# Kernel tuning notes

Measured on AMD Instinct MI355X. Metric: run time of the kernel, lower is better.

Reference implementation:

```python
import jax, jax.numpy as jnp
import numpy as np

N = 16384      # patches per slide
D = 1024       # inputd (hard-coded by attmil's Linear(1024, hd1))
HD = 512       # hd
HD2 = 256      # hd // 2
TOPK = 100     # torch.arange(100) after descending sort == top-100
R = 0.3
M_SEL = int(R * N)  # 4915 salient patches


def _l2norm(v, axis):
    # matches F.normalize(p=2, eps=1e-12)
    return v / jnp.maximum(jnp.linalg.norm(v, axis=axis, keepdims=True), 1e-12)


def setup_inputs() -> dict:
    key = jax.random.key(0)
    ks = jax.random.split(key, 12)
    def p(k, shape, scale=0.02):
        return jax.random.normal(k, shape, dtype=jnp.float32) * scale
    return {
        "x0": jax.random.normal(ks[0], (1, N, D), dtype=jnp.float32),
        "x1": jax.random.normal(ks[1], (1, N, D), dtype=jnp.float32),
        "Wq": p(ks[2], (D, HD)),  "bq": jnp.zeros((HD,), jnp.float32),
        "Wk": p(ks[3], (D, HD)),  "bk": jnp.zeros((HD,), jnp.float32),
        "W1": p(ks[4], (D, HD)),  "b1": jnp.zeros((HD,), jnp.float32),
        "Wv": p(ks[5], (HD, HD2)), "bv": jnp.zeros((HD2,), jnp.float32),
        "Wu": p(ks[6], (HD, HD2)), "bu": jnp.zeros((HD2,), jnp.float32),
        "Wa": p(ks[7], (HD2, 1)),  "ba": jnp.zeros((1,), jnp.float32),
        "Wc": p(ks[8], (HD, 1)),   "bc": jnp.zeros((1,), jnp.float32),
    }


def reference(x0, x1, Wq, bq, Wk, bk, W1, b1, Wv, bv, Wu, bu, Wa, ba, Wc, bc):
    # query/key projections with tanh
    q = jnp.tanh(x0 @ Wq + bq)                       # [1, N, HD]
    k = jnp.tanh(x1 @ Wk + bk)                       # [1, N, HD]
    qn = _l2norm(q, -1)
    kn = _l2norm(k, -1)
    A = jnp.einsum('bnd,bmd->bnm', qn, kn)           # cosine sims [1, N, N]
    # descending sort + index_select(arange(100)) == top-100 per row
    topv, _ = jax.lax.top_k(A, TOPK)                 # [1, N, 100]
    A1 = jnp.mean(topv, axis=-1)                     # saliency [1, N]
    # ascending sort of saliency; take first M_SEL indices (batch 0)
    sortidx = jnp.argsort(A1[0])                     # [N]
    sel = sortidx[:M_SEL]                            # [M_SEL]
    sal = x0[:, sel, :]                              # gather [1, M_SEL, D]
    # gated-attention MIL (attmil)
    feat = jax.nn.relu(sal @ W1 + b1)                # [1, M, HD]
    av = jnp.tanh(feat @ Wv + bv)                    # [1, M, HD2]
    au = jax.nn.sigmoid(feat @ Wu + bu)              # [1, M, HD2]
    att = (av * au) @ Wa + ba                        # [1, M, 1]
    att = jax.nn.softmax(att.transpose(0, 2, 1), axis=2)  # [1, 1, M]
    Mv = (att @ feat).reshape(-1, HD)                # [1, HD]
    Y_prob = Mv @ Wc + bc                            # [1, 1]
    return Y_prob, att
```

## Files before the change

kernel.cpp:

```cpp
#include <hip/hip_runtime.h>

typedef unsigned short u16;
typedef unsigned int u32;
typedef unsigned long long u64;

typedef __attribute__((ext_vector_type(8))) short bf16x8;
typedef __attribute__((ext_vector_type(4))) float f32x4;

__device__ __forceinline__ u16 f2b(float f) {
  u32 u = __float_as_uint(f);
  u32 r = (u + 0x7fffu + ((u >> 16) & 1u)) >> 16;
  return (u16)r;
}
__device__ __forceinline__ float b2f(u16 h) {
  return __uint_as_float(((u32)h) << 16);
}
__device__ __forceinline__ float key2f(u32 k) {
  u16 kk = (u16)k;
  u16 bits = (kk & 0x8000) ? (u16)(kk ^ 0x8000) : (u16)(~kk);
  return b2f(bits);
}
__device__ __forceinline__ u64 makekey(float f, int i) {
  u32 u = __float_as_uint(f);
  u = (u & 0x80000000u) ? ~u : (u | 0x80000000u);
  return ((u64)u << 32) | (u32)i;
}

__device__ __forceinline__ void gload16(const void* g, void* l) {
  __builtin_amdgcn_global_load_lds((const __attribute__((address_space(1))) void*)g,
                                   (__attribute__((address_space(3))) void*)l, 16, 0, 0);
}

__global__ __launch_bounds__(256) void conv_k(const float* __restrict__ s,
                                              u16* __restrict__ d, int n8) {
  int i = blockIdx.x * 256 + threadIdx.x;
  if (i >= n8) return;
  const float4* s4 = reinterpret_cast<const float4*>(s);
  float4 f0 = s4[i * 2], f1 = s4[i * 2 + 1];
  __align__(16) u16 t[8];
  t[0] = f2b(f0.x); t[1] = f2b(f0.y); t[2] = f2b(f0.z); t[3] = f2b(f0.w);
  t[4] = f2b(f1.x); t[5] = f2b(f1.y); t[6] = f2b(f1.z); t[7] = f2b(f1.w);
  reinterpret_cast<uint4*>(d)[i] = *reinterpret_cast<uint4*>(t);
}

__global__ __launch_bounds__(256) void convt_k(const float* __restrict__ W,
                                               u16* __restrict__ Wt, int K, int Nc) {
  __shared__ float t[32][33];
  int k0 = blockIdx.x * 32, n0 = blockIdx.y * 32;
  int c = threadIdx.x & 31, r4 = threadIdx.x >> 5;
#pragma unroll
  for (int i = 0; i < 4; ++i) {
    int r = r4 + i * 8;
    t[r][c] = W[(size_t)(k0 + r) * Nc + n0 + c];
  }
  __syncthreads();
#pragma unroll
  for (int i = 0; i < 4; ++i) {
    int r = r4 + i * 8;
    Wt[(size_t)(n0 + r) * K + k0 + c] = f2b(t[c][r]);
  }
}

template <int MODE>
__global__ __launch_bounds__(512, 2) void mm8_k(
    const u16* __restrict__ A, const u16* __restrict__ B, int K, int Mbase,
    int mtiles, const float* __restrict__ rs, const float* __restrict__ cs,
    const float* __restrict__ bias, u16* __restrict__ out, int ldc) {
  __shared__ u16 lds[2][2][2][128][32];
  int tid = threadIdx.x, lane = tid & 63, wid = tid >> 6;
  int wm = wid >> 2, wn = wid & 3;
  int rsel = lane & 15, rgrp = lane >> 4;

  int nwg = gridDim.x * gridDim.y;
  int fid = blockIdx.y * gridDim.x + blockIdx.x;
  int chunk = nwg >> 3;
  int s = (fid & 7) * chunk + (fid >> 3);
  int mtile = s % mtiles, ntile = s / mtiles;
  int mrow0 = Mbase + mtile * 256;
  int ncol0 = ntile * 256;

  int strow = wid * 16 + (lane >> 2);
  int stch = (lane & 3) ^ ((lane >> 3) & 3);

  auto stage = [&](int sbuf, int smat, int shalf, int kt) {
    int grow = (smat ? ncol0 : mrow0) + shalf * 128 + strow;
    const u16* g = (smat ? B : A) + (size_t)grow * K + kt * 32 + stch * 8;
    gload16(g, &lds[sbuf][smat][shalf][wid * 16][0]);
  };

  f32x4 acc[4][4][2] = {};
  bf16x8 afr[4], bfr[2][2];

  auto rdA = [&](int buf, int ah) {
#pragma unroll
    for (int mf = 0; mf < 4; ++mf) {
      int row = wm * 64 + mf * 16 + rsel;
      afr[mf] = *reinterpret_cast<const bf16x8*>(
          &lds[buf][0][ah][row][(rgrp ^ ((row >> 1) & 3)) * 8]);
    }
  };
  auto rdB = [&](int buf) {
#pragma unroll
    for (int bh = 0; bh < 2; ++bh)
#pragma unroll
      for (int nf = 0; nf < 2; ++nf) {
        int row = wn * 32 + nf * 16 + rsel;
        bfr[bh][nf] = *reinterpret_cast<const bf16x8*>(
            &lds[buf][1][bh][row][(rgrp ^ ((row >> 1) & 3)) * 8]);
      }
  };
  auto mm = [&](int ah) {
#pragma unroll
    for (int bh = 0; bh < 2; ++bh)
#pragma unroll
      for (int mf = 0; mf < 4; ++mf)
#pragma unroll
        for (int nf = 0; nf < 2; ++nf)
          acc[ah * 2 + bh][mf][nf] = __builtin_amdgcn_mfma_f32_16x16x32_bf16(
              afr[mf], bfr[bh][nf], acc[ah * 2 + bh][mf][nf], 0, 0, 0);
  };

  int nkt = K / 32;
  stage(0, 0, 0, 0); stage(0, 1, 0, 0); stage(0, 1, 1, 0); stage(0, 0, 1, 0);
  stage(1, 0, 0, 1); stage(1, 1, 0, 1);
  asm volatile("s_waitcnt vmcnt(2)" ::: "memory");
  __builtin_amdgcn_s_barrier();

  for (int j = 0; j < nkt / 2; ++j) {
    int t1 = 2 * j + 1;
    int t2 = (2 * j + 2 < nkt) ? 2 * j + 2 : nkt - 1;
    int t3 = (2 * j + 3 < nkt) ? 2 * j + 3 : nkt - 1;
    rdB(0); rdA(0, 0);
    stage(1, 1, 1, t1); stage(1, 0, 1, t1);
    __builtin_amdgcn_s_setprio(1); mm(0); __builtin_amdgcn_s_setprio(0);
    __builtin_amdgcn_s_barrier();
    rdA(0, 1);
    stage(0, 0, 0, t2); stage(0, 1, 0, t2);
    __builtin_amdgcn_s_setprio(1); mm(1); __builtin_amdgcn_s_setprio(0);
    asm volatile("s_waitcnt vmcnt(2)" ::: "memory");
    __builtin_amdgcn_s_barrier();
    rdB(1); rdA(1, 0);
    stage(0, 1, 1, t2); stage(0, 0, 1, t2);
    __builtin_amdgcn_s_setprio(1); mm(0); __builtin_amdgcn_s_setprio(0);
    __builtin_amdgcn_s_barrier();
    rdA(1, 1);
    stage(1, 0, 0, t3); stage(1, 1, 0, t3);
    __builtin_amdgcn_s_setprio(1); mm(1); __builtin_amdgcn_s_setprio(0);
    asm volatile("s_waitcnt vmcnt(2)" ::: "memory");
    __builtin_amdgcn_s_barrier();
  }

#pragma unroll
  for (int q = 0; q < 4; ++q)
#pragma unroll
    for (int mf = 0; mf < 4; ++mf)
#pragma unroll
      for (int nf = 0; nf < 2; ++nf)
#pragma unroll
        for (int r = 0; r < 4; ++r) {
          int rl = mtile * 256 + (q >> 1) * 128 + wm * 64 + mf * 16 + rgrp * 4 + r;
          int cl = ncol0 + (q & 1) * 128 + wn * 32 + nf * 16 + rsel;
          float v = acc[q][mf][nf][r] * rs[Mbase + rl] * cs[cl];
          out[(size_t)rl * ldc + cl] = f2b(v);
        }
}

__global__ __launch_bounds__(512, 2) void mm8p_k(
    const u16* __restrict__ A, const u16* __restrict__ B, int K, int mtiles,
    const float* __restrict__ bias, u16* __restrict__ out, int ldc,
    const u16* A2, const u16* B2, const float* bias2, u16* out2) {
  if (blockIdx.z) { A = A2; B = B2; bias = bias2; out = out2; }
  __shared__ u16 lds[3][3][128][32];
  int tid = threadIdx.x, lane = tid & 63, wid = tid >> 6;
  int wm = wid >> 2, wn = wid & 3;
  int rsel = lane & 15, rgrp = lane >> 4;

  int nwg = gridDim.x * gridDim.y;
  int fid = blockIdx.y * gridDim.x + blockIdx.x;
  int chunk = nwg >> 3;
  int s = (fid & 7) * chunk + (fid >> 3);
  int mtile = s % mtiles, ntile = s / mtiles;
  int mrow0 = mtile * 128;
  int ncol0 = ntile * 256;

  int strow = wid * 16 + (lane >> 2);
  int stch = (lane & 3) ^ ((lane >> 3) & 3);

  auto stage = [&](int sbuf, int slot, int kt) {
    int grow = (slot == 0 ? mrow0 : ncol0 + (slot - 1) * 128) + strow;
    const u16* g = (slot == 0 ? A : B) + (size_t)grow * K + kt * 32 + stch * 8;
    gload16(g, &lds[sbuf][slot][wid * 16][0]);
  };

  f32x4 acc[2][4][2] = {};
  bf16x8 afr[4], bfr[2][2];

  auto rdAll = [&](int buf) {
#pragma unroll
    for (int mf = 0; mf < 4; ++mf) {
      int row = wm * 64 + mf * 16 + rsel;
      afr[mf] = *reinterpret_cast<const bf16x8*>(
          &lds[buf][0][row][(rgrp ^ ((row >> 1) & 3)) * 8]);
    }
#pragma unroll
    for (int bh = 0; bh < 2; ++bh)
#pragma unroll
      for (int nf = 0; nf < 2; ++nf) {
        int row = wn * 32 + nf * 16 + rsel;
        bfr[bh][nf] = *reinterpret_cast<const bf16x8*>(
            &lds[buf][1 + bh][row][(rgrp ^ ((row >> 1) & 3)) * 8]);
      }
  };
  auto mm16 = [&]() {
#pragma unroll
    for (int bh = 0; bh < 2; ++bh)
#pragma unroll
      for (int mf = 0; mf < 4; ++mf)
#pragma unroll
        for (int nf = 0; nf < 2; ++nf)
          acc[bh][mf][nf] = __builtin_amdgcn_mfma_f32_16x16x32_bf16(
              afr[mf], bfr[bh][nf], acc[bh][mf][nf], 0, 0, 0);
  };

  int nkt = K / 32;
  stage(0, 0, 0); stage(0, 1, 0); stage(0, 2, 0);
  stage(1, 0, 1); stage(1, 1, 1); stage(1, 2, 1);
  asm volatile("s_waitcnt vmcnt(3)" ::: "memory");
  __builtin_amdgcn_s_barrier();

  int cur = 0;
  for (int t = 0; t < nkt; ++t) {
    rdAll(cur);
    int tn = (t + 2 < nkt) ? t + 2 : nkt - 1;
    int nb = cur + 2; if (nb >= 3) nb -= 3;
    stage(nb, 0, tn); stage(nb, 1, tn); stage(nb, 2, tn);
    __builtin_amdgcn_s_setprio(1); mm16(); __builtin_amdgcn_s_setprio(0);
    asm volatile("s_waitcnt vmcnt(3)" ::: "memory");
    __builtin_amdgcn_s_barrier();
    cur = (cur + 1 == 3) ? 0 : cur + 1;
  }

#pragma unroll
  for (int bh = 0; bh < 2; ++bh)
#pragma unroll
    for (int mf = 0; mf < 4; ++mf)
#pragma unroll
      for (int nf = 0; nf < 2; ++nf)
#pragma unroll
        for (int r = 0; r < 4; ++r) {
          int rl = mrow0 + wm * 64 + mf * 16 + rgrp * 4 + r;
          int cl = ncol0 + bh * 128 + wn * 32 + nf * 16 + rsel;
          float v = tanhf(acc[bh][mf][nf][r] + bias[cl]);
          out[(size_t)rl * ldc + cl] = f2b(v);
        }
}

#define TILE 128
#define BK 32

template <int MODE>
__global__ __launch_bounds__(256) void gemm2_k(
    const u16* __restrict__ Abf, const u16* __restrict__ Bbf, int lda, int ldb,
    int K, int Mreal, const float* __restrict__ bias,
    const u32* __restrict__ gidx, float* __restrict__ outf,
    u16* __restrict__ outb, int ldc,
    const u16* Abf2, const u16* Bbf2, const float* bias2,
    float* outf2, u16* outb2) {
  if (blockIdx.z) {
    if (Abf2) Abf = Abf2;
    if (Bbf2) Bbf = Bbf2;
    if (bias2) bias = bias2;
    if (outf2) outf = outf2;
    if (outb2) outb = outb2;
  }
  __shared__ u16 As[2][TILE][BK];
  __shared__ u16 Bs[2][TILE][BK];
  int tid = threadIdx.x, lane = tid & 63, wid = tid >> 6;
  int mt = blockIdx.x, nt2 = blockIdx.y;
  int row0 = (wid >> 1) * 64, col0 = (wid & 1) * 64;

  int scol = (lane & 3) * 8;
  const u16* gA[2];
  const u16* gB[2];
#pragma unroll
  for (int h = 0; h < 2; ++h) {
    int rA = (wid * 2 + h) * 16 + (lane >> 2);
    int grow = mt * TILE + rA;
    int arow;
    if (MODE == 2) arow = (int)gidx[grow < Mreal ? grow : 0];
    else arow = grow;
    gA[h] = Abf + (size_t)arow * lda + scol;
    int bcol = nt2 * TILE + rA;
    gB[h] = Bbf + (size_t)bcol * ldb + scol;
  }

  auto stage = [&](int buf, int kt) {
#pragma unroll
    for (int h = 0; h < 2; ++h) {
      gload16(gA[h] + kt, &As[buf][(wid * 2 + h) * 16][0]);
      gload16(gB[h] + kt, &Bs[buf][(wid * 2 + h) * 16][0]);
    }
  };

  f32x4 acc[4][4] = {};
  int k8 = 8 * (lane >> 4), rsel = lane & 15;
  int nkt = K / BK;

  stage(0, 0);
  __syncthreads();
  int cur = 0;
  for (int t = 0; t < nkt; ++t) {
    if (t + 1 < nkt) stage(cur ^ 1, (t + 1) * BK);
    bf16x8 a[4], b[4];
#pragma unroll
    for (int m = 0; m < 4; ++m)
      a[m] = *reinterpret_cast<const bf16x8*>(&As[cur][row0 + m * 16 + rsel][k8]);
#pragma unroll
    for (int n = 0; n < 4; ++n)
      b[n] = *reinterpret_cast<const bf16x8*>(&Bs[cur][col0 + n * 16 + rsel][k8]);
    __builtin_amdgcn_s_setprio(1);
#pragma unroll
    for (int m = 0; m < 4; ++m)
#pragma unroll
      for (int n = 0; n < 4; ++n)
        acc[m][n] = __builtin_amdgcn_mfma_f32_16x16x32_bf16(a[m], b[n], acc[m][n], 0, 0, 0);
    __builtin_amdgcn_s_setprio(0);
    __syncthreads();
    cur ^= 1;
  }

  int rgrp = lane >> 4, csel = lane & 15;
#pragma unroll
  for (int m = 0; m < 4; ++m)
#pragma unroll
    for (int n = 0; n < 4; ++n)
#pragma unroll
      for (int r = 0; r < 4; ++r) {
        int grow = mt * TILE + row0 + m * 16 + rgrp * 4 + r;
        int gcol = nt2 * TILE + col0 + n * 16 + csel;
        float v = acc[m][n][r];
        if (MODE == 2) {
          if (grow < Mreal) {
            v = fmaxf(v + bias[gcol], 0.f);
            outf[(size_t)grow * ldc + gcol] = v;
            outb[(size_t)grow * ldc + gcol] = f2b(v);
          }
        } else {
          if (grow < Mreal) outf[(size_t)grow * ldc + gcol] = v + bias[gcol];
        }
      }
}

__global__ __launch_bounds__(256) void norm_k(const u16* __restrict__ qb,
                                              float* __restrict__ inv, int rows, int dcols) {
  int gw = (int)((blockIdx.x * 256 + threadIdx.x) >> 6);
  int lane = threadIdx.x & 63;
  if (gw >= rows) return;
  const u16* r = qb + (size_t)gw * dcols;
  float s = 0.f;
  for (int c = lane; c < dcols; c += 64) { float v = b2f(r[c]); s += v * v; }
  for (int o = 32; o; o >>= 1) s += __shfl_down(s, o);
  if (lane == 0) inv[gw] = 1.f / fmaxf(sqrtf(s), 1e-12f);
}

__global__ __launch_bounds__(256) void topk_k(const u16* __restrict__ Ablk,
                                              float* __restrict__ A1, int rowbase) {
  __shared__ u32 hist[16][257];
  __shared__ u32 histlo[8][257];
  __shared__ u32 chist[256];
  __shared__ u32 sfx[257];
  __shared__ float wsfx[257];
  __shared__ float wsum[4];
  __shared__ int s_bhi;
  __shared__ u32 s_above;
  __shared__ float s_tail;
  int row = blockIdx.x, tid = threadIdx.x, wid = tid >> 6, lane = tid & 63;
  const uint4* src4 = reinterpret_cast<const uint4*>(Ablk + (size_t)row * 16384);
  uint4 regs[8];
#pragma unroll
  for (int v = 0; v < 8; ++v) regs[v] = src4[v * 256 + tid];
  for (int i = tid; i < 16 * 257; i += 256) (&hist[0][0])[i] = 0;
  for (int i = tid; i < 8 * 257; i += 256) (&histlo[0][0])[i] = 0;
#pragma unroll
  for (int v = 0; v < 8; ++v) {
    u32* w = reinterpret_cast<u32*>(&regs[v]);
#pragma unroll
    for (int h = 0; h < 4; ++h) {
      u32 x = w[h];
      u16 lo = (u16)x, hi = (u16)(x >> 16);
      lo = (lo & 0x8000) ? (u16)(~lo) : (u16)(lo | 0x8000);
      hi = (hi & 0x8000) ? (u16)(~hi) : (u16)(hi | 0x8000);
      w[h] = (u32)lo | ((u32)hi << 16);
    }
  }
  __syncthreads();

  u32* myh = &hist[lane & 15][0];
#pragma unroll
  for (int v = 0; v < 8; ++v) {
    const u32* w = reinterpret_cast<const u32*>(&regs[v]);
#pragma unroll
    for (int h = 0; h < 4; ++h) {
      atomicAdd(&myh[(w[h] >> 8) & 0xffu], 1u);
      atomicAdd(&myh[w[h] >> 24], 1u);
    }
  }
  __syncthreads();
  {
    u32 c = 0;
#pragma unroll
    for (int j = 0; j < 16; ++j) c += hist[j][tid];
    sfx[tid] = c;
    if (tid == 0) sfx[256] = 0;
  }
  __syncthreads();
#pragma unroll
  for (int st = 1; st < 256; st <<= 1) {
    u32 add = (tid + st < 256) ? sfx[tid + st] : 0u;
    __syncthreads();
    sfx[tid] += add;
    __syncthreads();
  }
  if (sfx[tid] >= 100u && sfx[tid + 1] < 100u) {
    s_bhi = tid;
    s_above = sfx[tid + 1];
  }
  __syncthreads();
  u32 bhi = (u32)s_bhi, above = s_above;

  u32* myl = &histlo[lane & 7][0];
  float lsum = 0.f;
#pragma unroll
  for (int v = 0; v < 8; ++v) {
    const u32* w = reinterpret_cast<const u32*>(&regs[v]);
#pragma unroll
    for (int h = 0; h < 4; ++h) {
#pragma unroll
      for (int half = 0; half < 2; ++half) {
        u32 k = (w[h] >> (half * 16)) & 0xffffu;
        u32 hb = k >> 8;
        if (hb > bhi) lsum += key2f(k);
        else if (hb == bhi) atomicAdd(&myl[k & 0xffu], 1u);
      }
    }
  }
  for (int o = 32; o; o >>= 1) lsum += __shfl_down(lsum, o);
  if (lane == 0) wsum[wid] = lsum;
  __syncthreads();
  {
    u32 c = 0;
#pragma unroll
    for (int j = 0; j < 8; ++j) c += histlo[j][tid];
    chist[tid] = c;
    sfx[tid] = c;
    wsfx[tid] = (float)c * key2f((bhi << 8) | (u32)tid);
    if (tid == 0) { sfx[256] = 0; wsfx[256] = 0.f; }
  }
  __syncthreads();
#pragma unroll
  for (int st = 1; st < 256; st <<= 1) {
    u32 a = (tid + st < 256) ? sfx[tid + st] : 0u;
    float b = (tid + st < 256) ? wsfx[tid + st] : 0.f;
    __syncthreads();
    sfx[tid] += a;
    wsfx[tid] += b;
    __syncthreads();
  }
  {
    u32 need = 100u - above;
    if (sfx[tid] >= need && sfx[tid + 1] < need) {
      s_tail = wsfx[tid + 1] +
               (float)(need - sfx[tid + 1]) * key2f((bhi << 8) | (u32)tid);
    }
  }
  __syncthreads();
  if (tid == 0) {
    float tot = wsum[0] + wsum[1] + wsum[2] + wsum[3];
    A1[rowbase + row] = (tot + s_tail) * 0.01f;
  }
}

__global__ __launch_bounds__(256) void rankpart_k(const float* __restrict__ A1,
                                                  u32* __restrict__ rank) {
  __shared__ u64 tile[2048];
  int i = blockIdx.x * 256 + threadIdx.x;
  int t0 = blockIdx.y * 2048;
  u64 my = makekey(A1[i], i);
  for (int j = threadIdx.x; j < 2048; j += 256) tile[j] = makekey(A1[t0 + j], t0 + j);
  __syncthreads();
  u32 r = 0;
  for (int j = 0; j < 2048; ++j) r += (tile[j] < my) ? 1u : 0u;
  atomicAdd(&rank[i], r);
}

__global__ __launch_bounds__(256) void scatter_k(const u32* __restrict__ rank,
                                                 u32* __restrict__ sortidx) {
  int i = blockIdx.x * 256 + threadIdx.x;
  sortidx[rank[i]] = (u32)i;
}

__global__ __launch_bounds__(256) void attlogit_k(const float* __restrict__ avr,
                                                  const float* __restrict__ aur,
                                                  const float* __restrict__ featf,
                                                  const float* __restrict__ Wa,
                                                  const float* __restrict__ Wc,
                                                  float* __restrict__ z, float* __restrict__ g,
                                                  int M) {
  int gw = (int)((blockIdx.x * 256 + threadIdx.x) >> 6);
  int lane = threadIdx.x & 63;
  if (gw >= M) return;
  float s = 0.f;
  for (int c = lane; c < 256; c += 64) {
    float a = tanhf(avr[(size_t)gw * 256 + c]);
    float u = 1.f / (1.f + expf(-aur[(size_t)gw * 256 + c]));
    s += a * u * Wa[c];
  }
  float t = 0.f;
  for (int c = lane; c < 512; c += 64) t += featf[(size_t)gw * 512 + c] * Wc[c];
  for (int o = 32; o; o >>= 1) {
    s += __shfl_down(s, o);
    t += __shfl_down(t, o);
  }
  if (lane == 0) {
    z[gw] = s;
    g[gw] = t;
  }
}

__global__ __launch_bounds__(1024) void final_k(const float* __restrict__ z,
                                                const float* __restrict__ g,
                                                const float* __restrict__ bc,
                                                float* __restrict__ out, int M) {
  __shared__ float sred[16], s1[16], s2[16];
  int tid = threadIdx.x, lane = tid & 63, w = tid >> 6;
  float m = -1e30f;
  for (int i = tid; i < M; i += 1024) m = fmaxf(m, z[i]);
  for (int o = 32; o; o >>= 1) m = fmaxf(m, __shfl_down(m, o));
  if (lane == 0) sred[w] = m;
  __syncthreads();
  if (w == 0) {
    float t = (lane < 16) ? sred[lane] : -1e30f;
    for (int o = 8; o; o >>= 1) t = fmaxf(t, __shfl_down(t, o));
    if (lane == 0) sred[0] = t;
  }
  __syncthreads();
  m = sred[0];
  float se = 0.f, sg = 0.f;
  for (int i = tid; i < M; i += 1024) {
    float e = expf(z[i] - m);
    se += e;
    sg += e * g[i];
  }
  for (int o = 32; o; o >>= 1) {
    se += __shfl_down(se, o);
    sg += __shfl_down(sg, o);
  }
  if (lane == 0) {
    s1[w] = se;
    s2[w] = sg;
  }
  __syncthreads();
  if (w == 0) {
    float a = (lane < 16) ? s1[lane] : 0.f;
    float b = (lane < 16) ? s2[lane] : 0.f;
    for (int o = 8; o; o >>= 1) {
      a += __shfl_down(a, o);
      b += __shfl_down(b, o);
    }
    if (lane == 0) {
      s1[0] = a;
      s2[0] = b;
    }
  }
  __syncthreads();
  float inv = 1.f / s1[0];
  for (int i = tid; i < M; i += 1024) out[1 + i] = expf(z[i] - m) * inv;
  if (tid == 0) out[0] = s2[0] * inv + bc[0];
}

extern "C" void kernel_launch(void* const* d_in, const int* in_sizes, int n_in,
                              void* d_out, int out_size, void* d_ws, size_t ws_size,
                              hipStream_t stream) {
  const int N = 16384, D = 1024, HD = 512, HD2 = 256, MSEL = 4915;
  const float* x0 = (const float*)d_in[0];
  const float* x1 = (const float*)d_in[1];
  const float* Wq = (const float*)d_in[2];
  const float* bq = (const float*)d_in[3];
  const float* Wk = (const float*)d_in[4];
  const float* bk = (const float*)d_in[5];
  const float* W1 = (const float*)d_in[6];
  const float* b1 = (const float*)d_in[7];
  const float* Wv = (const float*)d_in[8];
  const float* bv = (const float*)d_in[9];
  const float* Wu = (const float*)d_in[10];
  const float* bu = (const float*)d_in[11];
  const float* Wa = (const float*)d_in[12];
  const float* Wc = (const float*)d_in[14];
  const float* bc = (const float*)d_in[15];
  float* out = (float*)d_out;

  char* base = (char*)d_ws;
  size_t off = 0;
  auto alloc = [&](size_t b) {
    void* r = base + off;
    off = (off + b + 255) & ~(size_t)255;
    return r;
  };
  const int MPAD = 4992;
  u16* wqt = (u16*)alloc((size_t)HD * D * 2);
  u16* wkt = (u16*)alloc((size_t)HD * D * 2);
  u16* w1t = (u16*)alloc((size_t)HD * D * 2);
  u16* wvt = (u16*)alloc((size_t)HD2 * HD * 2);
  u16* wut = (u16*)alloc((size_t)HD2 * HD * 2);
  u16* x0b = (u16*)alloc((size_t)N * D * 2);
  u16* x1b = (u16*)alloc((size_t)N * D * 2);
  u16* qb = (u16*)alloc((size_t)N * HD * 2);
  u16* kb = (u16*)alloc((size_t)N * HD * 2);
  float* invq = (float*)alloc((size_t)N * 4);
  float* invk = (float*)alloc((size_t)N * 4);
  float* A1 = (float*)alloc((size_t)N * 4);
  u32* rankbuf = (u32*)alloc((size_t)N * 4);
  u32* sortidx = (u32*)alloc((size_t)N * 4);
  float* featf = (float*)alloc((size_t)MPAD * HD * 4);
  u16* featb = (u16*)alloc((size_t)MPAD * HD * 2);
  float* avr = (float*)alloc((size_t)MPAD * HD2 * 4);
  float* aur = (float*)alloc((size_t)MPAD * HD2 * 4);
  float* zbuf = (float*)alloc((size_t)MPAD * 4);
  float* gbuf = (float*)alloc((size_t)MPAD * 4);
  const int ablk = 2048;
  u16* Ablk = (u16*)alloc((size_t)ablk * N * 2);

  conv_k<<<(N * D / 8 + 255) / 256, 256, 0, stream>>>(x0, x0b, N * D / 8);
  conv_k<<<(N * D / 8 + 255) / 256, 256, 0, stream>>>(x1, x1b, N * D / 8);
  convt_k<<<dim3(D / 32, HD / 32), 256, 0, stream>>>(Wq, wqt, D, HD);
  convt_k<<<dim3(D / 32, HD / 32), 256, 0, stream>>>(Wk, wkt, D, HD);
  convt_k<<<dim3(D / 32, HD / 32), 256, 0, stream>>>(W1, w1t, D, HD);
  convt_k<<<dim3(HD / 32, HD2 / 32), 256, 0, stream>>>(Wv, wvt, HD, HD2);
  convt_k<<<dim3(HD / 32, HD2 / 32), 256, 0, stream>>>(Wu, wut, HD, HD2);

  mm8p_k<<<dim3(4, 64, 2), 512, 0, stream>>>(
      x0b, wqt, D, 128, bq, qb, HD, x1b, wkt, bk, kb);

  norm_k<<<N / 4, 256, 0, stream>>>(qb, invq, N, HD);
  norm_k<<<N / 4, 256, 0, stream>>>(kb, invk, N, HD);

  for (int it = 0; it < N / ablk; ++it) {
    mm8_k<1><<<dim3(8, 64), 512, 0, stream>>>(
        qb, kb, HD, it * ablk, 8, invq, invk, nullptr, Ablk, N);
    topk_k<<<ablk, 256, 0, stream>>>(Ablk, A1, it * ablk);
  }

  hipMemsetAsync(rankbuf, 0, (size_t)N * 4, stream);
  rankpart_k<<<dim3(N / 256, 8), 256, 0, stream>>>(A1, rankbuf);
  scatter_k<<<N / 256, 256, 0, stream>>>(rankbuf, sortidx);

  gemm2_k<2><<<dim3((MSEL + TILE - 1) / TILE, HD / TILE), 256, 0, stream>>>(
      x0b, w1t, D, D, D, MSEL, b1, sortidx, featf, featb, HD,
      nullptr, nullptr, nullptr, nullptr, nullptr);

  gemm2_k<3><<<dim3((MSEL + TILE - 1) / TILE, HD2 / TILE, 2), 256, 0, stream>>>(
      featb, wvt, HD, HD, HD, MSEL, bv, nullptr, avr, nullptr, HD2,
      nullptr, wut, bu, aur, nullptr);

  attlogit_k<<<(MSEL + 3) / 4, 256, 0, stream>>>(avr, aur, featf, Wa, Wc, zbuf, gbuf, MSEL);

  final_k<<<1, 1024, 0, stream>>>(zbuf, gbuf, bc, out, MSEL);
}
```

Measured before the change: 808.2 us.

## Unify GEMM kernels with simpler full-tile double-buffered main loop

```diff
diff --git a/kernel.cpp b/kernel.cpp
--- a/kernel.cpp
+++ b/kernel.cpp
@@ -62,10 +62,12 @@
 }
 
 template <int MODE>
-__global__ __launch_bounds__(512, 2) void mm8_k(
+__global__ __launch_bounds__(512, 2) void mmF_k(
     const u16* __restrict__ A, const u16* __restrict__ B, int K, int Mbase,
     int mtiles, const float* __restrict__ rs, const float* __restrict__ cs,
-    const float* __restrict__ bias, u16* __restrict__ out, int ldc) {
+    const float* __restrict__ bias, u16* __restrict__ out, int ldc,
+    const u16* A2, const u16* B2, const float* bias2, u16* out2) {
+  if (MODE == 0 && blockIdx.z) { A = A2; B = B2; bias = bias2; out = out2; }
   __shared__ u16 lds[2][2][2][128][32];
   int tid = threadIdx.x, lane = tid & 63, wid = tid >> 6;
   int wm = wid >> 2, wn = wid & 3;
@@ -87,19 +89,23 @@
     const u16* g = (smat ? B : A) + (size_t)grow * K + kt * 32 + stch * 8;
     gload16(g, &lds[sbuf][smat][shalf][wid * 16][0]);
   };
+  auto stage4 = [&](int sbuf, int kt) {
+    stage(sbuf, 0, 0, kt); stage(sbuf, 1, 0, kt);
+    stage(sbuf, 0, 1, kt); stage(sbuf, 1, 1, kt);
+  };
 
   f32x4 acc[4][4][2] = {};
-  bf16x8 afr[4], bfr[2][2];
-
-  auto rdA = [&](int buf, int ah) {
-#pragma unroll
-    for (int mf = 0; mf < 4; ++mf) {
-      int row = wm * 64 + mf * 16 + rsel;
-      afr[mf] = *reinterpret_cast<const bf16x8*>(
-          &lds[buf][0][ah][row][(rgrp ^ ((row >> 1) & 3)) * 8]);
-    }
-  };
-  auto rdB = [&](int buf) {
+  bf16x8 afr[2][4], bfr[2][2];
+
+  auto rdAll = [&](int buf) {
+#pragma unroll
+    for (int ah = 0; ah < 2; ++ah)
+#pragma unroll
+      for (int mf = 0; mf < 4; ++mf) {
+        int row = wm * 64 + mf * 16 + rsel;
+        afr[ah][mf] = *reinterpret_cast<const bf16x8*>(
+            &lds[buf][0][ah][row][(rgrp ^ ((row >> 1) & 3)) * 8]);
+      }
 #pragma unroll
     for (int bh = 0; bh < 2; ++bh)
 #pragma unroll
@@ -109,44 +115,36 @@
             &lds[buf][1][bh][row][(rgrp ^ ((row >> 1) & 3)) * 8]);
       }
   };
-  auto mm = [&](int ah) {
-#pragma unroll
-    for (int bh = 0; bh < 2; ++bh)
-#pragma unroll
-      for (int mf = 0; mf < 4; ++mf)
-#pragma unroll
-        for (int nf = 0; nf < 2; ++nf)
-          acc[ah * 2 + bh][mf][nf] = __builtin_amdgcn_mfma_f32_16x16x32_bf16(
-              afr[mf], bfr[bh][nf], acc[ah * 2 + bh][mf][nf], 0, 0, 0);
+  auto mm32 = [&]() {
+#pragma unroll
+    for (int ah = 0; ah < 2; ++ah)
+#pragma unroll
+      for (int bh = 0; bh < 2; ++bh)
+#pragma unroll
+        for (int mf = 0; mf < 4; ++mf)
+#pragma unroll
+          for (int nf = 0; nf < 2; ++nf)
+            acc[ah * 2 + bh][mf][nf] = __builtin_amdgcn_mfma_f32_16x16x32_bf16(
+                afr[ah][mf], bfr[bh][nf], acc[ah * 2 + bh][mf][nf], 0, 0, 0);
   };
 
   int nkt = K / 32;
-  stage(0, 0, 0, 0); stage(0, 1, 0, 0); stage(0, 1, 1, 0); stage(0, 0, 1, 0);
-  stage(1, 0, 0, 1); stage(1, 1, 0, 1);
-  asm volatile("s_waitcnt vmcnt(2)" ::: "memory");
+  stage4(0, 0);
+  stage4(1, 1);
+  asm volatile("s_waitcnt vmcnt(4)" ::: "memory");
   __builtin_amdgcn_s_barrier();
 
-  for (int j = 0; j < nkt / 2; ++j) {
-    int t1 = 2 * j + 1;
-    int t2 = (2 * j + 2 < nkt) ? 2 * j + 2 : nkt - 1;
-    int t3 = (2 * j + 3 < nkt) ? 2 * j + 3 : nkt - 1;
-    rdB(0); rdA(0, 0);
-    stage(1, 1, 1, t1); stage(1, 0, 1, t1);
-    __builtin_amdgcn_s_setprio(1); mm(0); __builtin_amdgcn_s_setprio(0);
+  for (int t = 0; t < nkt; ++t) {
+    int buf = t & 1;
+    rdAll(buf);
+    asm volatile("s_waitcnt lgkmcnt(0)" ::: "memory");
     __builtin_amdgcn_s_barrier();
-    rdA(0, 1);
-    stage(0, 0, 0, t2); stage(0, 1, 0, t2);
-    __builtin_amdgcn_s_setprio(1); mm(1); __builtin_amdgcn_s_setprio(0);
-    asm volatile("s_waitcnt vmcnt(2)" ::: "memory");
-    __builtin_amdgcn_s_barrier();
-    rdB(1); rdA(1, 0);
-    stage(0, 1, 1, t2); stage(0, 0, 1, t2);
-    __builtin_amdgcn_s_setprio(1); mm(0); __builtin_amdgcn_s_setprio(0);
-    __builtin_amdgcn_s_barrier();
-    rdA(1, 1);
-    stage(1, 0, 0, t3); stage(1, 1, 0, t3);
-    __builtin_amdgcn_s_setprio(1); mm(1); __builtin_amdgcn_s_setprio(0);
-    asm volatile("s_waitcnt vmcnt(2)" ::: "memory");
+    int t2 = (t + 2 < nkt) ? t + 2 : nkt - 1;
+    stage4(buf, t2);
+    __builtin_amdgcn_s_setprio(1);
+    mm32();
+    __builtin_amdgcn_s_setprio(0);
+    asm volatile("s_waitcnt vmcnt(4)" ::: "memory");
     __builtin_amdgcn_s_barrier();
   }
 
@@ -160,97 +158,9 @@
         for (int r = 0; r < 4; ++r) {
           int rl = mtile * 256 + (q >> 1) * 128 + wm * 64 + mf * 16 + rgrp * 4 + r;
           int cl = ncol0 + (q & 1) * 128 + wn * 32 + nf * 16 + rsel;
-          float v = acc[q][mf][nf][r] * rs[Mbase + rl] * cs[cl];
-          out[(size_t)rl * ldc + cl] = f2b(v);
-        }
-}
-
-__global__ __launch_bounds__(512, 2) void mm8p_k(
-    const u16* __restrict__ A, const u16* __restrict__ B, int K, int mtiles,
-    const float* __restrict__ bias, u16* __restrict__ out, int ldc,
-    const u16* A2, const u16* B2, const float* bias2, u16* out2) {
-  if (blockIdx.z) { A = A2; B = B2; bias = bias2; out = out2; }
-  __shared__ u16 lds[3][3][128][32];
-  int tid = threadIdx.x, lane = tid & 63, wid = tid >> 6;
-  int wm = wid >> 2, wn = wid & 3;
-  int rsel = lane & 15, rgrp = lane >> 4;
-
-  int nwg = gridDim.x * gridDim.y;
-  int fid = blockIdx.y * gridDim.x + blockIdx.x;
-  int chunk = nwg >> 3;
-  int s = (fid & 7) * chunk + (fid >> 3);
-  int mtile = s % mtiles, ntile = s / mtiles;
-  int mrow0 = mtile * 128;
-  int ncol0 = ntile * 256;
-
-  int strow = wid * 16 + (lane >> 2);
-  int stch = (lane & 3) ^ ((lane >> 3) & 3);
-
-  auto stage = [&](int sbuf, int slot, int kt) {
-    int grow = (slot == 0 ? mrow0 : ncol0 + (slot - 1) * 128) + strow;
-    const u16* g = (slot == 0 ? A : B) + (size_t)grow * K + kt * 32 + stch * 8;
-    gload16(g, &lds[sbuf][slot][wid * 16][0]);
-  };
-
-  f32x4 acc[2][4][2] = {};
-  bf16x8 afr[4], bfr[2][2];
-
-  auto rdAll = [&](int buf) {
-#pragma unroll
-    for (int mf = 0; mf < 4; ++mf) {
-      int row = wm * 64 + mf * 16 + rsel;
-      afr[mf] = *reinterpret_cast<const bf16x8*>(
-          &lds[buf][0][row][(rgrp ^ ((row >> 1) & 3)) * 8]);
-    }
-#pragma unroll
-    for (int bh = 0; bh < 2; ++bh)
-#pragma unroll
-      for (int nf = 0; nf < 2; ++nf) {
-        int row = wn * 32 + nf * 16 + rsel;
-        bfr[bh][nf] = *reinterpret_cast<const bf16x8*>(
-            &lds[buf][1 + bh][row][(rgrp ^ ((row >> 1) & 3)) * 8]);
-      }
-  };
-  auto mm16 = [&]() {
-#pragma unroll
-    for (int bh = 0; bh < 2; ++bh)
-#pragma unroll
-      for (int mf = 0; mf < 4; ++mf)
-#pragma unroll
-        for (int nf = 0; nf < 2; ++nf)
-          acc[bh][mf][nf] = __builtin_amdgcn_mfma_f32_16x16x32_bf16(
-              afr[mf], bfr[bh][nf], acc[bh][mf][nf], 0, 0, 0);
-  };
-
-  int nkt = K / 32;
-  stage(0, 0, 0); stage(0, 1, 0); stage(0, 2, 0);
-  stage(1, 0, 1); stage(1, 1, 1); stage(1, 2, 1);
-  asm volatile("s_waitcnt vmcnt(3)" ::: "memory");
-  __builtin_amdgcn_s_barrier();
-
-  int cur = 0;
-  for (int t = 0; t < nkt; ++t) {
-    rdAll(cur);
-    int tn = (t + 2 < nkt) ? t + 2 : nkt - 1;
-    int nb = cur + 2; if (nb >= 3) nb -= 3;
-    stage(nb, 0, tn); stage(nb, 1, tn); stage(nb, 2, tn);
-    __builtin_amdgcn_s_setprio(1); mm16(); __builtin_amdgcn_s_setprio(0);
-    asm volatile("s_waitcnt vmcnt(3)" ::: "memory");
-    __builtin_amdgcn_s_barrier();
-    cur = (cur + 1 == 3) ? 0 : cur + 1;
-  }
-
-#pragma unroll
-  for (int bh = 0; bh < 2; ++bh)
-#pragma unroll
-    for (int mf = 0; mf < 4; ++mf)
-#pragma unroll
-      for (int nf = 0; nf < 2; ++nf)
-#pragma unroll
-        for (int r = 0; r < 4; ++r) {
-          int rl = mrow0 + wm * 64 + mf * 16 + rgrp * 4 + r;
-          int cl = ncol0 + bh * 128 + wn * 32 + nf * 16 + rsel;
-          float v = tanhf(acc[bh][mf][nf][r] + bias[cl]);
+          float v = acc[q][mf][nf][r];
+          if (MODE == 1) v *= rs[Mbase + rl] * cs[cl];
+          else v = tanhf(v + bias[cl]);
           out[(size_t)rl * ldc + cl] = f2b(v);
         }
 }
@@ -638,15 +548,17 @@
   convt_k<<<dim3(HD / 32, HD2 / 32), 256, 0, stream>>>(Wv, wvt, HD, HD2);
   convt_k<<<dim3(HD / 32, HD2 / 32), 256, 0, stream>>>(Wu, wut, HD, HD2);
 
-  mm8p_k<<<dim3(4, 64, 2), 512, 0, stream>>>(
-      x0b, wqt, D, 128, bq, qb, HD, x1b, wkt, bk, kb);
+  mmF_k<0><<<dim3(2, 64, 2), 512, 0, stream>>>(
+      x0b, wqt, D, 0, 64, nullptr, nullptr, bq, qb, HD,
+      x1b, wkt, bk, kb);
 
   norm_k<<<N / 4, 256, 0, stream>>>(qb, invq, N, HD);
   norm_k<<<N / 4, 256, 0, stream>>>(kb, invk, N, HD);
 
   for (int it = 0; it < N / ablk; ++it) {
-    mm8_k<1><<<dim3(8, 64), 512, 0, stream>>>(
-        qb, kb, HD, it * ablk, 8, invq, invk, nullptr, Ablk, N);
+    mmF_k<1><<<dim3(8, 64), 512, 0, stream>>>(
+        qb, kb, HD, it * ablk, 8, invq, invk, nullptr, Ablk, N,
+        nullptr, nullptr, nullptr, nullptr);
     topk_k<<<ablk, 256, 0, stream>>>(Ablk, A1, it * ablk);
   }
 
```

Result: slower. 898.3 us (+11.1%).
